# Kernel optimization log

Hardware: AMD Instinct MI355X
Metric: run time of the kernel (lower is better)

## Reference

```python
import jax, jax.numpy as jnp
import numpy as np

SIZES = [128, 64, 32, 16, 8]   # H=W per pyramid level
REFINE = 2                     # gather/refine level -> 32x32
C = 256
GROUPS = 32                    # dim_out // 8
EPS = 1e-5


def _maxpool(x, k):
    # exact adaptive_max_pool2d when input size is divisible by output size
    if k == 1:
        return x
    return jax.lax.reduce_window(x, -jnp.inf, jax.lax.max,
                                 (1, 1, k, k), (1, 1, k, k), 'VALID')


def _upsample(x, f):
    # nearest-neighbor interpolate with exact integer scale factor
    if f == 1:
        return x
    return jnp.repeat(jnp.repeat(x, f, axis=2), f, axis=3)


def _conv1x1(x, w, b):
    return jnp.einsum('nchw,oc->nohw', x, w) + b[None, :, None, None]


def _group_norm(x, gamma, beta):
    n, c, h, w = x.shape
    xg = x.reshape(n, GROUPS, c // GROUPS, h, w)
    mu = xg.mean(axis=(2, 3, 4), keepdims=True)
    var = xg.var(axis=(2, 3, 4), keepdims=True)
    xg = (xg - mu) * jax.lax.rsqrt(var + EPS)
    return xg.reshape(n, c, h, w) * gamma[None, :, None, None] + beta[None, :, None, None]


def _nonlocal(x, g_w, g_b, th_w, th_b, ph_w, ph_b, out_w, out_b, gn_g, gn_b):
    n, c, h, w = x.shape
    N = h * w
    g_x = _conv1x1(x, g_w, g_b).reshape(n, c, N)       # [n,c,N]
    th_x = _conv1x1(x, th_w, th_b).reshape(n, c, N)
    ph_x = _conv1x1(x, ph_w, ph_b).reshape(n, c, N)
    # pairwise = theta^T @ phi / N  (dot_product mode, no softmax)
    pw = jnp.einsum('nci,ncj->nij', th_x, ph_x) / N    # [n,N,N]
    y = jnp.einsum('nij,ncj->nci', pw, g_x)            # [n,c,N]
    y = y.reshape(n, c, h, w)
    out = _group_norm(_conv1x1(y, out_w, out_b), gn_g, gn_b)
    return x + out


def reference(f0, f1, f2, f3, f4,
              g_w, g_b, th_w, th_b, ph_w, ph_b,
              out_w, out_b, gn_g, gn_b):
    feats = [f0, f1, f2, f3, f4]
    gs = SIZES[REFINE]
    gathered = []
    for i, f in enumerate(feats):
        if i < REFINE:
            gathered.append(_maxpool(f, SIZES[i] // gs))
        else:
            gathered.append(_upsample(f, gs // SIZES[i]))
    bsf = sum(gathered) / len(gathered)
    bsf = _nonlocal(bsf, g_w, g_b, th_w, th_b, ph_w, ph_b, out_w, out_b, gn_g, gn_b)
    outs = []
    for i, f in enumerate(feats):
        if i < REFINE:
            res = _upsample(bsf, SIZES[i] // gs)
        else:
            res = _maxpool(bsf, gs // SIZES[i])
        outs.append(res + f)
    return tuple(outs)


def setup_inputs() -> dict:
    key = jax.random.key(0)
    ks = jax.random.split(key, 16)
    inp = {}
    for i, s in enumerate(SIZES):
        inp[f'f{i}'] = jax.random.normal(ks[i], (4, C, s, s), dtype=jnp.float32)
    std = 0.01
    inp['g_w'] = jax.random.normal(ks[5], (C, C), dtype=jnp.float32) * std
    inp['g_b'] = jnp.zeros((C,), jnp.float32)
    inp['th_w'] = jax.random.normal(ks[6], (C, C), dtype=jnp.float32) * std
    inp['th_b'] = jnp.zeros((C,), jnp.float32)
    inp['ph_w'] = jax.random.normal(ks[7], (C, C), dtype=jnp.float32) * std
    inp['ph_b'] = jnp.zeros((C,), jnp.float32)
    inp['out_w'] = jax.random.normal(ks[8], (C, C), dtype=jnp.float32) * std
    inp['out_b'] = jnp.zeros((C,), jnp.float32)
    inp['gn_g'] = jnp.ones((C,), jnp.float32)
    inp['gn_b'] = jnp.zeros((C,), jnp.float32)
    return inp
```

## Files before the change

### kernel.cpp

```cpp
#include <hip/hip_runtime.h>

typedef __bf16 bf16x8 __attribute__((ext_vector_type(8)));
typedef float f32x4 __attribute__((ext_vector_type(4)));

#define OFF_BSF   0x000000
#define OFF_BSFT  0x400000
#define OFF_BSFB  0x600000
#define OFF_YT    0x600000
#define OFF_Z     0x800000
#define OFF_SBH   0xC00000
#define OFF_SBL   0xC80000
#define OFF_T0    0xD00000
#define OFF_OWB   0xE00000
#define OFF_GWT   0xE20000
#define OFF_PHT   0xE40000
#define OFF_THT   0xE60000
#define OFF_UB    0xE80000
#define OFF_VB    0xEA0000
#define OFF_UT    0xEC0000
#define OFF_RPART 0xEE0000
#define OFF_R     0xEF0000
#define OFF_UV    0xEF1000
#define OFF_V2P   0xEF1400
#define OFF_W2P   0xEF2400
#define OFF_S2    0xEF3400
#define OFF_CVEC  0xEF4000
#define OFF_STATS 0xEF9000
#define OFF_W2SP  0xEFA000

__global__ __launch_bounds__(256) void prep_k(
    const float* __restrict__ f0, const float* __restrict__ f1,
    const float* __restrict__ f2, const float* __restrict__ f3,
    const float* __restrict__ f4,
    const float* __restrict__ g_w, const float* __restrict__ ph_w,
    const float* __restrict__ th_w, const float* __restrict__ ow_w,
    const float* __restrict__ g_b, const float* __restrict__ ph_b,
    const float* __restrict__ th_b,
    char* __restrict__ ws)
{
  const int blk = blockIdx.x, t = threadIdx.x;
  __shared__ __attribute__((aligned(16))) union {
    __bf16 Lt[16][66];
    __bf16 T[64][72];
    float vec2[544];
  } sm;

  if (blk < 48) {
    const int w = blk >> 4, tl = blk & 15;
    const float* src = (w == 0) ? g_w : (w == 1) ? ph_w : th_w;
    __bf16* dst = (__bf16*)(ws + ((w == 0) ? OFF_GWT : (w == 1) ? OFF_PHT : OFF_THT));
    const int ti = (tl >> 2) * 64, tj = (tl & 3) * 64;
#pragma unroll
    for (int i = 0; i < 4; ++i) {
      int idx = i * 256 + t;
      int r = idx >> 4, c4 = (idx & 15) << 2;
      float4 v = *(const float4*)&src[(size_t)(ti + r) * 256 + tj + c4];
      sm.T[c4 + 0][r] = (__bf16)v.x;
      sm.T[c4 + 1][r] = (__bf16)v.y;
      sm.T[c4 + 2][r] = (__bf16)v.z;
      sm.T[c4 + 3][r] = (__bf16)v.w;
    }
    __syncthreads();
#pragma unroll
    for (int i = 0; i < 2; ++i) {
      int idx = i * 256 + t;
      int aa = idx >> 3, cc = (idx & 7) << 3;
      bf16x8 o = *(const bf16x8*)&sm.T[aa][cc];
      *(bf16x8*)&dst[(size_t)(tj + aa) * 256 + ti + cc] = o;
    }
  } else if (blk < 52) {
    const int r0 = (blk - 48) * 64;
    __bf16* owB = (__bf16*)(ws + OFF_OWB);
#pragma unroll
    for (int i = 0; i < 8; ++i) {
      int lin = i * 2048 + t * 8;
      size_t gidx = (size_t)r0 * 256 + lin;
      float4 v0 = *(const float4*)&ow_w[gidx];
      float4 v1 = *(const float4*)&ow_w[gidx + 4];
      bf16x8 o;
      o[0] = (__bf16)v0.x; o[1] = (__bf16)v0.y; o[2] = (__bf16)v0.z; o[3] = (__bf16)v0.w;
      o[4] = (__bf16)v1.x; o[5] = (__bf16)v1.y; o[6] = (__bf16)v1.z; o[7] = (__bf16)v1.w;
      *(bf16x8*)&owB[gidx] = o;
    }
  } else if (blk < 68) {
    const int q = blk - 52;
    const int r0 = q * 16;
    float* uv = (float*)(ws + OFF_UV);
    sm.vec2[t] = g_b[t];
    __syncthreads();
    const int rl = t >> 4;
    const int ci = (t & 15) * 16;
    const float* p = ow_w + (size_t)(r0 + rl) * 256 + ci;
    float acc = 0.f;
#pragma unroll
    for (int u = 0; u < 4; ++u) {
      float4 v = *(const float4*)(p + u * 4);
      acc += v.x * sm.vec2[ci + u * 4]     + v.y * sm.vec2[ci + u * 4 + 1]
           + v.z * sm.vec2[ci + u * 4 + 2] + v.w * sm.vec2[ci + u * 4 + 3];
    }
    __syncthreads();
    sm.vec2[256 + rl * 17 + (t & 15)] = acc;
    __syncthreads();
    if (t < 16) {
      float s = 0.f;
#pragma unroll
      for (int i = 0; i < 16; ++i) s += sm.vec2[256 + t * 17 + i];
      uv[r0 + t] = s;
    }
  } else if (blk < 72) {
    const int q = blk - 68, c0 = q * 64;
    float* v2p = (float*)(ws + OFF_V2P);
    if (t < 64) sm.vec2[t] = th_b[c0 + t];
    __syncthreads();
    float acc = 0.f;
#pragma unroll 8
    for (int c = 0; c < 64; ++c)
      acc += ph_w[(size_t)(c0 + c) * 256 + t] * sm.vec2[c];
    v2p[q * 256 + t] = acc;
  } else if (blk < 76) {
    const int q = blk - 72, c0 = q * 64;
    float* w2p = (float*)(ws + OFF_W2P);
    if (t < 64) sm.vec2[t] = ph_b[c0 + t];
    __syncthreads();
    float acc = 0.f;
#pragma unroll 8
    for (int c = 0; c < 64; ++c)
      acc += th_w[(size_t)(c0 + c) * 256 + t] * sm.vec2[c];
    w2p[q * 256 + t] = acc;
  } else if (blk == 76) {
    float* s2 = (float*)(ws + OFF_S2);
    if (t < 64) {
      float pa = ph_b[t] * th_b[t] + ph_b[64 + t] * th_b[64 + t]
               + ph_b[128 + t] * th_b[128 + t] + ph_b[192 + t] * th_b[192 + t];
#pragma unroll
      for (int off = 32; off; off >>= 1) pa += __shfl_down(pa, off);
      if (t == 0) s2[0] = pa;
    }
    ((float*)(ws + OFF_STATS))[t] = 0.f;
  } else if (blk == 77) {
    float* cvec = (float*)(ws + OFF_CVEC);
#pragma unroll
    for (int i = 0; i < 4; ++i) cvec[i * 256 + t] = 0.f;
  } else {
    const int g = blk - 78;
    float*  bsf   = (float*)(ws + OFF_BSF);
    __bf16* bsfT  = (__bf16*)(ws + OFF_BSFT);
    __bf16* bsfB  = (__bf16*)(ws + OFF_BSFB);
    float*  rpart = (float*)(ws + OFF_RPART);
    const int sblk = g & 15, cgrp = (g >> 4) & 15, b = g >> 8;
    const int c0 = cgrp * 16, s0 = sblk * 64;
    const int spl = t & 63, sp = s0 + spl;
    const int y = sp >> 5, x = sp & 31;
#pragma unroll
    for (int i = 0; i < 4; ++i) {
      const int cl = (t >> 6) + i * 4;
      const int nc = b * 256 + c0 + cl;

      const float* p0 = f0 + (size_t)nc * 16384 + (y * 4) * 128 + x * 4;
      float4 r0 = *(const float4*)(p0);
      float4 r1 = *(const float4*)(p0 + 128);
      float4 r2 = *(const float4*)(p0 + 256);
      float4 r3 = *(const float4*)(p0 + 384);
      float a  = fmaxf(fmaxf(r0.x, r0.y), fmaxf(r0.z, r0.w));
      float bb = fmaxf(fmaxf(r1.x, r1.y), fmaxf(r1.z, r1.w));
      float c  = fmaxf(fmaxf(r2.x, r2.y), fmaxf(r2.z, r2.w));
      float d  = fmaxf(fmaxf(r3.x, r3.y), fmaxf(r3.z, r3.w));
      float m0v = fmaxf(fmaxf(a, bb), fmaxf(c, d));

      const float* p1 = f1 + (size_t)nc * 4096 + (y * 2) * 64 + x * 2;
      float2 s0v = *(const float2*)(p1);
      float2 s1v = *(const float2*)(p1 + 64);
      float m1v = fmaxf(fmaxf(s0v.x, s0v.y), fmaxf(s1v.x, s1v.y));

      float v2 = f2[(size_t)nc * 1024 + sp];
      float v3 = f3[(size_t)nc * 256 + (y >> 1) * 16 + (x >> 1)];
      float v4 = f4[(size_t)nc * 64  + (y >> 2) * 8  + (x >> 2)];
      float val = (m0v + m1v + v2 + v3 + v4) * 0.2f;
      bsf[(size_t)nc * 1024 + sp]  = val;
      bsfB[(size_t)nc * 1024 + sp] = (__bf16)val;
      sm.Lt[cl][spl] = (__bf16)val;
      float rs = val;
#pragma unroll
      for (int off = 32; off; off >>= 1) rs += __shfl_down(rs, off);
      if (spl == 0) rpart[sblk * 1024 + nc] = rs;
    }
    __syncthreads();
#pragma unroll
    for (int i = 0; i < 4; ++i) {
      int linear = t + i * 256;
      int spl2 = linear >> 4, cl2 = linear & 15;
      bsfT[((size_t)b * 1024 + s0 + spl2) * 256 + c0 + cl2] = sm.Lt[cl2][spl2];
    }
  }
}

__device__ __forceinline__ void gemm_acc(
    const __bf16* __restrict__ A, const __bf16* __restrict__ B,
    const int K, const int m0, const int n0,
    __bf16 (*Al)[64][72], __bf16 (*Bl)[64][72],
    f32x4 acc[2][2])
{
  const int t = threadIdx.x;
  const int lane = t & 63, wv = t >> 6;
  const int wm = (wv & 1) * 32, wn = (wv >> 1) * 32;
  const int fr = lane & 15, lk = (lane >> 4) * 8;
  const int sr = t >> 2, sk = (t & 3) * 16;

  const __bf16* Ar = A + (size_t)(m0 + sr) * K + sk;
  const __bf16* Br = B + (size_t)(n0 + sr) * K + sk;

  bf16x8 ra0 = *(const bf16x8*)(Ar);
  bf16x8 ra1 = *(const bf16x8*)(Ar + 8);
  bf16x8 rb0 = *(const bf16x8*)(Br);
  bf16x8 rb1 = *(const bf16x8*)(Br + 8);

  const int nIter = K >> 6;
  int p = 0;
  for (int it = 0; it < nIter; ++it) {
    *(bf16x8*)&Al[p][sr][sk]     = ra0;
    *(bf16x8*)&Al[p][sr][sk + 8] = ra1;
    *(bf16x8*)&Bl[p][sr][sk]     = rb0;
    *(bf16x8*)&Bl[p][sr][sk + 8] = rb1;
    __syncthreads();
    if (it + 1 < nIter) {
      const __bf16* An = Ar + (size_t)(it + 1) * 64;
      const __bf16* Bn = Br + (size_t)(it + 1) * 64;
      ra0 = *(const bf16x8*)(An);
      ra1 = *(const bf16x8*)(An + 8);
      rb0 = *(const bf16x8*)(Bn);
      rb1 = *(const bf16x8*)(Bn + 8);
    }
#pragma unroll
    for (int kk = 0; kk < 64; kk += 32) {
      bf16x8 a0 = *(const bf16x8*)&Al[p][wm + fr][kk + lk];
      bf16x8 a1 = *(const bf16x8*)&Al[p][wm + 16 + fr][kk + lk];
      bf16x8 b0 = *(const bf16x8*)&Bl[p][wn + fr][kk + lk];
      bf16x8 b1 = *(const bf16x8*)&Bl[p][wn + 16 + fr][kk + lk];
      acc[0][0] = __builtin_amdgcn_mfma_f32_16x16x32_bf16(a0, b0, acc[0][0], 0, 0, 0);
      acc[0][1] = __builtin_amdgcn_mfma_f32_16x16x32_bf16(a0, b1, acc[0][1], 0, 0, 0);
      acc[1][0] = __builtin_amdgcn_mfma_f32_16x16x32_bf16(a1, b0, acc[1][0], 0, 0, 0);
      acc[1][1] = __builtin_amdgcn_mfma_f32_16x16x32_bf16(a1, b1, acc[1][1], 0, 0, 0);
    }
    __syncthreads();
    p ^= 1;
  }
}

__device__ __forceinline__ void store_bf16(
    __bf16* dst, int ldst, const f32x4 acc[2][2],
    int m0, int n0, int wm, int wn, int rbase, int fr)
{
#pragma unroll
  for (int i = 0; i < 2; ++i)
#pragma unroll
    for (int r = 0; r < 4; ++r) {
      int m = m0 + wm + i * 16 + rbase + r;
#pragma unroll
      for (int j = 0; j < 2; ++j) {
        int n = n0 + wn + j * 16 + fr;
        dst[(size_t)m * ldst + n] = (__bf16)acc[i][j][r];
      }
    }
}

#define ZERO_ACC(acc) \
  _Pragma("unroll") for (int i_ = 0; i_ < 2; ++i_) \
  _Pragma("unroll") for (int j_ = 0; j_ < 2; ++j_) \
    acc[i_][j_] = (f32x4){0.f, 0.f, 0.f, 0.f};

__global__ __launch_bounds__(256) void p0_k(char* __restrict__ ws)
{
  const int blk = blockIdx.x, t = threadIdx.x;
  __shared__ __attribute__((aligned(16))) __bf16 Al[2][64][72];
  __shared__ __attribute__((aligned(16))) __bf16 Bl[2][64][72];
  float* shf = (float*)(&Al[0][0][0]);

  const int lane = t & 63, wv = t >> 6;
  const int wm = (wv & 1) * 32, wn = (wv >> 1) * 32;
  const int fr = lane & 15, rbase = (lane >> 4) * 4;
  (void)lane; (void)wv;

  const __bf16* bsfB = (const __bf16*)(ws + OFF_BSFB);

  if (blk < 64) {
    const int b = blk >> 4, tl = blk & 15;
    const int m0 = (tl >> 2) * 64, n0 = (tl & 3) * 64;
    f32x4 acc[2][2]; ZERO_ACC(acc);
    gemm_acc(bsfB + (size_t)b * 262144, bsfB + (size_t)b * 262144,
             1024, m0, n0, Al, Bl, acc);
    __bf16* oh = (__bf16*)(ws + OFF_SBH) + (size_t)b * 65536;
    __bf16* ol = (__bf16*)(ws + OFF_SBL) + (size_t)b * 65536;
#pragma unroll
    for (int i = 0; i < 2; ++i)
#pragma unroll
      for (int r = 0; r < 4; ++r) {
        int m = m0 + wm + i * 16 + rbase + r;
#pragma unroll
        for (int j = 0; j < 2; ++j) {
          int n = n0 + wn + j * 16 + fr;
          float v = acc[i][j][r];
          __bf16 h = (__bf16)v;
          oh[(size_t)m * 256 + n] = h;
          ol[(size_t)m * 256 + n] = (__bf16)(v - (float)h);
        }
      }
  } else if (blk < 80) {
    const int tl = blk - 64;
    const int m0 = (tl >> 2) * 64, n0 = (tl & 3) * 64;
    f32x4 acc[2][2]; ZERO_ACC(acc);
    gemm_acc((const __bf16*)(ws + OFF_OWB), (const __bf16*)(ws + OFF_GWT),
             256, m0, n0, Al, Bl, acc);
    __bf16* ub = (__bf16*)(ws + OFF_UB);
    __bf16* ut = (__bf16*)(ws + OFF_UT);
#pragma unroll
    for (int i = 0; i < 2; ++i)
#pragma unroll
      for (int r = 0; r < 4; ++r) {
        int m = m0 + wm + i * 16 + rbase + r;
#pragma unroll
        for (int j = 0; j < 2; ++j) {
          int n = n0 + wn + j * 16 + fr;
          __bf16 v = (__bf16)acc[i][j][r];
          ub[(size_t)m * 256 + n] = v;
          ut[(size_t)n * 256 + m] = v;
        }
      }
  } else if (blk < 96) {
    const int tl = blk - 80;
    const int m0 = (tl >> 2) * 64, n0 = (tl & 3) * 64;
    f32x4 acc[2][2]; ZERO_ACC(acc);
    gemm_acc((const __bf16*)(ws + OFF_PHT), (const __bf16*)(ws + OFF_THT),
             256, m0, n0, Al, Bl, acc);
    store_bf16((__bf16*)(ws + OFF_VB), 256, acc, m0, n0, wm, wn, rbase, fr);
  } else if (blk == 96) {
    const float* rpart = (const float*)(ws + OFF_RPART);
    float* Rr = (float*)(ws + OFF_R);
#pragma unroll
    for (int j2 = 0; j2 < 4; ++j2) {
      int idx = t + j2 * 256;
      float s = 0.f;
#pragma unroll
      for (int k = 0; k < 16; ++k) s += rpart[k * 1024 + idx];
      Rr[idx] = s;
    }
  } else {
    const int q = blk - 97;
    const int half = q >> 4, idx = q & 15;
    const int b = idx >> 2, seg = (idx & 3) * 256;
    const int ch0 = half * 128;
    const float* w2p = (const float*)(ws + OFF_W2P);
    const float* bsf = (const float*)(ws + OFF_BSF);
    float* w2sp = (float*)(ws + OFF_W2SP);
    if (t < 128) {
      int c = ch0 + t;
      shf[t] = w2p[c] + w2p[256 + c] + w2p[512 + c] + w2p[768 + c];
    }
    __syncthreads();
    float acc = 0.f;
#pragma unroll 8
    for (int c = 0; c < 128; ++c)
      acc += shf[c] * bsf[((size_t)(b * 256 + ch0 + c)) * 1024 + seg + t];
    w2sp[half * 4096 + b * 1024 + seg + t] = acc;
  }
}

__global__ __launch_bounds__(256) void p1_k(char* __restrict__ ws)
{
  const int blk = blockIdx.x, t = threadIdx.x;
  __shared__ __attribute__((aligned(16))) __bf16 Al[2][64][72];
  __shared__ __attribute__((aligned(16))) __bf16 Bl[2][64][72];
  float* shf = (float*)(&Al[0][0][0]);

  const int lane = t & 63, wv = t >> 6;
  const int wm = (wv & 1) * 32, wn = (wv >> 1) * 32;
  const int fr = lane & 15, rbase = (lane >> 4) * 4;
  (void)lane; (void)wv;

  const __bf16* UB = (const __bf16*)(ws + OFF_UB);
  const float* Rr  = (const float*)(ws + OFF_R);
  const float* uv  = (const float*)(ws + OFF_UV);

  if (blk < 64) {
    const int b = blk >> 4, tl = blk & 15;
    const int m0 = (tl >> 2) * 64, n0 = (tl & 3) * 64;
    f32x4 acc[2][2]; ZERO_ACC(acc);
    gemm_acc(UB, (const __bf16*)(ws + OFF_SBH) + (size_t)b * 65536,
             256, m0, n0, Al, Bl, acc);
    gemm_acc(UB, (const __bf16*)(ws + OFF_SBL) + (size_t)b * 65536,
             256, m0, n0, Al, Bl, acc);
    shf[t] = Rr[b * 256 + t];
    __syncthreads();
    __bf16* od = (__bf16*)(ws + OFF_T0) + (size_t)b * 65536;
#pragma unroll
    for (int i = 0; i < 2; ++i)
#pragma unroll
      for (int r = 0; r < 4; ++r) {
        int m = m0 + wm + i * 16 + rbase + r;
        float uvm = uv[m];
#pragma unroll
        for (int j = 0; j < 2; ++j) {
          int n = n0 + wn + j * 16 + fr;
          od[(size_t)m * 256 + n] = (__bf16)(acc[i][j][r] + uvm * shf[n]);
        }
      }
  } else if (blk < 320) {
    const int q = blk - 64;
    const int b = q >> 6, tl = q & 63;
    const int m0 = (tl >> 2) * 64, n0 = (tl & 3) * 64;
    f32x4 acc[2][2]; ZERO_ACC(acc);
    gemm_acc((const __bf16*)(ws + OFF_BSFT) + (size_t)b * 262144,
             (const __bf16*)(ws + OFF_VB), 256, m0, n0, Al, Bl, acc);
    const float* v2p = (const float*)(ws + OFF_V2P);
    shf[t] = v2p[t] + v2p[256 + t] + v2p[512 + t] + v2p[768 + t];
    __syncthreads();
    __bf16* od = (__bf16*)(ws + OFF_YT) + (size_t)b * 262144;
#pragma unroll
    for (int i = 0; i < 2; ++i)
#pragma unroll
      for (int r = 0; r < 4; ++r) {
        int m = m0 + wm + i * 16 + rbase + r;
#pragma unroll
        for (int j = 0; j < 2; ++j) {
          int n = n0 + wn + j * 16 + fr;
          od[(size_t)m * 256 + n] = (__bf16)(acc[i][j][r] + shf[n]);
        }
      }
  } else {
    const int q = blk - 320;
    const int b = q >> 2, cc = (q & 3) * 64;
    const __bf16* UT = (const __bf16*)(ws + OFF_UT);
    float* cvec = (float*)(ws + OFF_CVEC);
    if (t < 64) shf[t] = Rr[b * 256 + cc + t];
    __syncthreads();
    float acc = 0.f;
#pragma unroll 8
    for (int c = 0; c < 64; ++c)
      acc += (float)UT[(size_t)(cc + c) * 256 + t] * shf[c];
    atomicAdd(&cvec[b * 256 + t], acc);
  }
}

__global__ __launch_bounds__(256) void p2_k(char* __restrict__ ws,
                                            const float* __restrict__ ow_b)
{
  const int blk = blockIdx.x, t = threadIdx.x;
  __shared__ __attribute__((aligned(16))) __bf16 Al[2][64][72];
  __shared__ __attribute__((aligned(16))) __bf16 Bl[2][64][72];
  float* shf = (float*)(&Al[0][0][0]);

  const int lane = t & 63, wv = t >> 6;
  const int wm = (wv & 1) * 32, wn = (wv >> 1) * 32;
  const int fr = lane & 15, rbase = (lane >> 4) * 4;

  const int b = blk >> 6, t6 = blk & 63;
  const int mt = t6 >> 4, nt = t6 & 15;
  const int m0 = mt * 64, n0 = nt * 64;
  (void)nt;

  f32x4 acc[2][2]; ZERO_ACC(acc);
  gemm_acc((const __bf16*)(ws + OFF_T0) + (size_t)b * 65536,
           (const __bf16*)(ws + OFF_YT) + (size_t)b * 262144,
           256, m0, n0, Al, Bl, acc);

  const float* uv   = (const float*)(ws + OFF_UV);
  const float* cvec = (const float*)(ws + OFF_CVEC);
  const float* w2sp = (const float*)(ws + OFF_W2SP);
  const float s2v   = *(const float*)(ws + OFF_S2);
  float* SRAW = (float*)(ws + OFF_STATS);
  float* zb = (float*)(ws + OFF_Z) + (size_t)b * 262144;

  float gs[2] = {0.f, 0.f}, gq[2] = {0.f, 0.f};
  int gidx[2];
  const float s1024 = 1.f / 1024.f;
#pragma unroll
  for (int i = 0; i < 2; ++i) {
    gidx[i] = (wm + i * 16 + rbase) >> 3;
#pragma unroll
    for (int r = 0; r < 4; ++r) {
      int m = m0 + wm + i * 16 + rbase + r;
      float coefm = uv[m] + cvec[b * 256 + m] * s1024;
      float qm = s2v * coefm + ow_b[m];
#pragma unroll
      for (int j = 0; j < 2; ++j) {
        int n = n0 + wn + j * 16 + fr;
        float w2n = w2sp[b * 1024 + n] + w2sp[4096 + b * 1024 + n];
        float v = acc[i][j][r] * s1024 + coefm * w2n + qm;
        zb[(size_t)m * 1024 + n] = v;
        gs[i] += v;
        gq[i] += v * v;
      }
    }
  }
  __syncthreads();
  if (t < 16) shf[t] = 0.f;
  __syncthreads();
#pragma unroll
  for (int i = 0; i < 2; ++i) {
    atomicAdd(&shf[gidx[i] * 2], gs[i]);
    atomicAdd(&shf[gidx[i] * 2 + 1], gq[i]);
  }
  __syncthreads();
  if (t < 16) {
    int g = mt * 8 + (t >> 1);
    atomicAdd(&SRAW[(b * 32 + g) * 2 + (t & 1)], shf[t]);
  }
}

__device__ __forceinline__ float4 gmix(float4 bz, float4 zz, float a, float c)
{
  float4 r;
  r.x = bz.x + zz.x * a + c;
  r.y = bz.y + zz.y * a + c;
  r.z = bz.z + zz.z * a + c;
  r.w = bz.w + zz.w * a + c;
  return r;
}
__device__ __forceinline__ float max4(float4 v)
{ return fmaxf(fmaxf(v.x, v.y), fmaxf(v.z, v.w)); }

__device__ __forceinline__ void gn_coeff(const float2* __restrict__ ST,
                                         const float* __restrict__ gamma,
                                         const float* __restrict__ beta,
                                         int b, int ch, float& a, float& c0)
{
  float2 sq = ST[b * 32 + (ch >> 3)];
  float mean = sq.x * (1.0f / 8192.0f);
  float var  = sq.y * (1.0f / 8192.0f) - mean * mean;
  float inv  = rsqrtf(var + 1e-5f);
  a  = inv * gamma[ch];
  c0 = beta[ch] - mean * a;
}

__global__ __launch_bounds__(256) void scat_k(
    const char* __restrict__ ws,
    const float* __restrict__ f0, const float* __restrict__ f1,
    const float* __restrict__ f2, const float* __restrict__ f3,
    const float* __restrict__ f4,
    const float* __restrict__ gamma, const float* __restrict__ beta,
    float* __restrict__ out)
{
  const float* Z = (const float*)(ws + OFF_Z);
  const float* BSF = (const float*)(ws + OFF_BSF);
  const float2* ST = (const float2*)(ws + OFF_STATS);
  const int i4 = blockIdx.x * 256 + threadIdx.x;

  if (i4 < 4194304) {
    const int l = i4 << 2;
    const int x = l & 127, yy = (l >> 7) & 127, nc = l >> 14;
    const int ch = nc & 255, b = nc >> 8;
    float a, c0; gn_coeff(ST, gamma, beta, b, ch, a, c0);
    size_t base = (size_t)nc * 1024 + ((yy >> 2) << 5) + (x >> 2);
    float v = BSF[base] + Z[base] * a + c0;
    float4 f = ((const float4*)f0)[i4];
    float4 o; o.x = f.x + v; o.y = f.y + v; o.z = f.z + v; o.w = f.w + v;
    ((float4*)out)[i4] = o;
  } else if (i4 < 5242880) {
    const int l4 = i4 - 4194304;
    const int l = l4 << 2;
    const int x = l & 63, yy = (l >> 6) & 63, nc = l >> 12;
    const int ch = nc & 255, b = nc >> 8;
    float a, c0; gn_coeff(ST, gamma, beta, b, ch, a, c0);
    size_t base = (size_t)nc * 1024 + ((yy >> 1) << 5) + (x >> 1);
    float v0 = BSF[base] + Z[base] * a + c0;
    float v1 = BSF[base + 1] + Z[base + 1] * a + c0;
    float4 f = ((const float4*)f1)[l4];
    float4 o; o.x = f.x + v0; o.y = f.y + v0; o.z = f.z + v1; o.w = f.w + v1;
    ((float4*)out)[i4] = o;
  } else if (i4 < 5505024) {
    const int l4 = i4 - 5242880;
    const int l = l4 << 2;
    const int nc = l >> 10, e = l & 1023;
    const int ch = nc & 255, b = nc >> 8;
    float a, c0; gn_coeff(ST, gamma, beta, b, ch, a, c0);
    size_t base = (size_t)nc * 1024 + e;
    float4 z4 = *(const float4*)&Z[base];
    float4 b4 = *(const float4*)&BSF[base];
    float4 v = gmix(b4, z4, a, c0);
    float4 f = ((const float4*)f2)[l4];
    float4 o; o.x = f.x + v.x; o.y = f.y + v.y; o.z = f.z + v.z; o.w = f.w + v.w;
    ((float4*)out)[i4] = o;
  } else if (i4 < 5570560) {
    const int l4 = i4 - 5505024;
    const int l = l4 << 2;
    const int x = l & 15, yy = (l >> 4) & 15, nc = l >> 8;
    const int ch = nc & 255, b = nc >> 8;
    float a, c0; gn_coeff(ST, gamma, beta, b, ch, a, c0);
    size_t base = (size_t)nc * 1024;
    const int p0 = (yy * 2) * 32 + (x * 2);
    float4 r0a = gmix(*(const float4*)&BSF[base + p0],      *(const float4*)&Z[base + p0],      a, c0);
    float4 r0b = gmix(*(const float4*)&BSF[base + p0 + 4],  *(const float4*)&Z[base + p0 + 4],  a, c0);
    float4 r1a = gmix(*(const float4*)&BSF[base + p0 + 32], *(const float4*)&Z[base + p0 + 32], a, c0);
    float4 r1b = gmix(*(const float4*)&BSF[base + p0 + 36], *(const float4*)&Z[base + p0 + 36], a, c0);
    float4 f = ((const float4*)f3)[l4];
    float4 o;
    o.x = f.x + fmaxf(fmaxf(r0a.x, r0a.y), fmaxf(r1a.x, r1a.y));
    o.y = f.y + fmaxf(fmaxf(r0a.z, r0a.w), fmaxf(r1a.z, r1a.w));
    o.z = f.z + fmaxf(fmaxf(r0b.x, r0b.y), fmaxf(r1b.x, r1b.y));
    o.w = f.w + fmaxf(fmaxf(r0b.z, r0b.w), fmaxf(r1b.z, r1b.w));
    ((float4*)out)[i4] = o;
  } else {
    const int l4 = i4 - 5570560;
    const int l = l4 << 2;
    const int x = l & 7, yy = (l >> 3) & 7, nc = l >> 6;
    const int ch = nc & 255, b = nc >> 8;
    float a, c0; gn_coeff(ST, gamma, beta, b, ch, a, c0);
    size_t base = (size_t)nc * 1024;
    float4 mx = {-3.4e38f, -3.4e38f, -3.4e38f, -3.4e38f};
#pragma unroll
    for (int r = 0; r < 4; ++r) {
      const float* zp = &Z[base + (size_t)(yy * 4 + r) * 32 + x * 4];
      const float* bp = &BSF[base + (size_t)(yy * 4 + r) * 32 + x * 4];
      float4 q0 = gmix(*(const float4*)(bp),      *(const float4*)(zp),      a, c0);
      float4 q1 = gmix(*(const float4*)(bp + 4),  *(const float4*)(zp + 4),  a, c0);
      float4 q2 = gmix(*(const float4*)(bp + 8),  *(const float4*)(zp + 8),  a, c0);
      float4 q3 = gmix(*(const float4*)(bp + 12), *(const float4*)(zp + 12), a, c0);
      mx.x = fmaxf(mx.x, max4(q0));
      mx.y = fmaxf(mx.y, max4(q1));
      mx.z = fmaxf(mx.z, max4(q2));
      mx.w = fmaxf(mx.w, max4(q3));
    }
    float4 f = ((const float4*)f4)[l4];
    float4 o; o.x = f.x + mx.x; o.y = f.y + mx.y; o.z = f.z + mx.z; o.w = f.w + mx.w;
    ((float4*)out)[i4] = o;
  }
}

extern "C" void kernel_launch(void* const* d_in, const int* in_sizes, int n_in,
                              void* d_out, int out_size, void* d_ws, size_t ws_size,
                              hipStream_t stream)
{
  (void)in_sizes; (void)n_in; (void)out_size; (void)ws_size;
  const float* f0   = (const float*)d_in[0];
  const float* f1   = (const float*)d_in[1];
  const float* f2   = (const float*)d_in[2];
  const float* f3   = (const float*)d_in[3];
  const float* f4   = (const float*)d_in[4];
  const float* g_w  = (const float*)d_in[5];
  const float* g_b  = (const float*)d_in[6];
  const float* th_w = (const float*)d_in[7];
  const float* th_b = (const float*)d_in[8];
  const float* ph_w = (const float*)d_in[9];
  const float* ph_b = (const float*)d_in[10];
  const float* ow_w = (const float*)d_in[11];
  const float* ow_b = (const float*)d_in[12];
  const float* gn_g = (const float*)d_in[13];
  const float* gn_b = (const float*)d_in[14];
  char* ws = (char*)d_ws;

  prep_k<<<1102, 256, 0, stream>>>(f0, f1, f2, f3, f4,
                                   g_w, ph_w, th_w, ow_w,
                                   g_b, ph_b, th_b, ws);
  p0_k<<<129, 256, 0, stream>>>(ws);
  p1_k<<<336, 256, 0, stream>>>(ws);
  p2_k<<<256, 256, 0, stream>>>(ws, ow_b);
  scat_k<<<21824, 256, 0, stream>>>(ws, f0, f1, f2, f3, f4, gn_g, gn_b,
                                    (float*)d_out);
}
```

Baseline: 85.36 us.

## Store bsf and pre-norm output intermediates in bf16 instead of fp32

Drops the fp32 copy of the gathered feature map and reads the existing bf16 copy in the w2sp reduction and the final scatter kernel. The pre-GroupNorm output Z is also written and read as bf16, so intermediate traffic in the last kernels is roughly halved. YT is moved to a new offset to avoid overlapping the bf16 buffers. The cost is reduced precision in the residual path and the GN input, which may increase error against the fp32 reference.

```diff
diff --git a/kernel.cpp b/kernel.cpp
--- a/kernel.cpp
+++ b/kernel.cpp
@@ -1,13 +1,12 @@
 #include <hip/hip_runtime.h>
 
 typedef __bf16 bf16x8 __attribute__((ext_vector_type(8)));
+typedef __bf16 bf16x4v __attribute__((ext_vector_type(4)));
 typedef float f32x4 __attribute__((ext_vector_type(4)));
 
-#define OFF_BSF   0x000000
 #define OFF_BSFT  0x400000
 #define OFF_BSFB  0x600000
-#define OFF_YT    0x600000
-#define OFF_Z     0x800000
+#define OFF_ZB    0x800000
 #define OFF_SBH   0xC00000
 #define OFF_SBL   0xC80000
 #define OFF_T0    0xD00000
@@ -27,6 +26,7 @@
 #define OFF_CVEC  0xEF4000
 #define OFF_STATS 0xEF9000
 #define OFF_W2SP  0xEFA000
+#define OFF_YT    0xF10000
 
 __global__ __launch_bounds__(256) void prep_k(
     const float* __restrict__ f0, const float* __restrict__ f1,
@@ -143,7 +143,6 @@
     for (int i = 0; i < 4; ++i) cvec[i * 256 + t] = 0.f;
   } else {
     const int g = blk - 78;
-    float*  bsf   = (float*)(ws + OFF_BSF);
     __bf16* bsfT  = (__bf16*)(ws + OFF_BSFT);
     __bf16* bsfB  = (__bf16*)(ws + OFF_BSFB);
     float*  rpart = (float*)(ws + OFF_RPART);
@@ -176,7 +175,6 @@
       float v3 = f3[(size_t)nc * 256 + (y >> 1) * 16 + (x >> 1)];
       float v4 = f4[(size_t)nc * 64  + (y >> 2) * 8  + (x >> 2)];
       float val = (m0v + m1v + v2 + v3 + v4) * 0.2f;
-      bsf[(size_t)nc * 1024 + sp]  = val;
       bsfB[(size_t)nc * 1024 + sp] = (__bf16)val;
       sm.Lt[cl][spl] = (__bf16)val;
       float rs = val;
@@ -349,7 +347,6 @@
     const int b = idx >> 2, seg = (idx & 3) * 256;
     const int ch0 = half * 128;
     const float* w2p = (const float*)(ws + OFF_W2P);
-    const float* bsf = (const float*)(ws + OFF_BSF);
     float* w2sp = (float*)(ws + OFF_W2SP);
     if (t < 128) {
       int c = ch0 + t;
@@ -359,7 +356,7 @@
     float acc = 0.f;
 #pragma unroll 8
     for (int c = 0; c < 128; ++c)
-      acc += shf[c] * bsf[((size_t)(b * 256 + ch0 + c)) * 1024 + seg + t];
+      acc += shf[c] * (float)bsfB[((size_t)(b * 256 + ch0 + c)) * 1024 + seg + t];
     w2sp[half * 4096 + b * 1024 + seg + t] = acc;
   }
 }
@@ -467,7 +464,7 @@
   const float* w2sp = (const float*)(ws + OFF_W2SP);
   const float s2v   = *(const float*)(ws + OFF_S2);
   float* SRAW = (float*)(ws + OFF_STATS);
-  float* zb = (float*)(ws + OFF_Z) + (size_t)b * 262144;
+  __bf16* zb = (__bf16*)(ws + OFF_ZB) + (size_t)b * 262144;
 
   float gs[2] = {0.f, 0.f}, gq[2] = {0.f, 0.f};
   int gidx[2];
@@ -485,7 +482,7 @@
         int n = n0 + wn + j * 16 + fr;
         float w2n = w2sp[b * 1024 + n] + w2sp[4096 + b * 1024 + n];
         float v = acc[i][j][r] * s1024 + coefm * w2n + qm;
-        zb[(size_t)m * 1024 + n] = v;
+        zb[(size_t)m * 1024 + n] = (__bf16)v;
         gs[i] += v;
         gq[i] += v * v;
       }
@@ -506,6 +503,11 @@
   }
 }
 
+__device__ __forceinline__ float4 b2f4(const __bf16* p)
+{
+  bf16x4v v = *(const bf16x4v*)p;
+  return (float4){(float)v[0], (float)v[1], (float)v[2], (float)v[3]};
+}
 __device__ __forceinline__ float4 gmix(float4 bz, float4 zz, float a, float c)
 {
   float4 r;
@@ -539,8 +541,8 @@
     const float* __restrict__ gamma, const float* __restrict__ beta,
     float* __restrict__ out)
 {
-  const float* Z = (const float*)(ws + OFF_Z);
-  const float* BSF = (const float*)(ws + OFF_BSF);
+  const __bf16* ZB  = (const __bf16*)(ws + OFF_ZB);
+  const __bf16* BSF = (const __bf16*)(ws + OFF_BSFB);
   const float2* ST = (const float2*)(ws + OFF_STATS);
   const int i4 = blockIdx.x * 256 + threadIdx.x;
 
@@ -550,7 +552,7 @@
     const int ch = nc & 255, b = nc >> 8;
     float a, c0; gn_coeff(ST, gamma, beta, b, ch, a, c0);
     size_t base = (size_t)nc * 1024 + ((yy >> 2) << 5) + (x >> 2);
-    float v = BSF[base] + Z[base] * a + c0;
+    float v = (float)BSF[base] + (float)ZB[base] * a + c0;
     float4 f = ((const float4*)f0)[i4];
     float4 o; o.x = f.x + v; o.y = f.y + v; o.z = f.z + v; o.w = f.w + v;
     ((float4*)out)[i4] = o;
@@ -561,8 +563,8 @@
     const int ch = nc & 255, b = nc >> 8;
     float a, c0; gn_coeff(ST, gamma, beta, b, ch, a, c0);
     size_t base = (size_t)nc * 1024 + ((yy >> 1) << 5) + (x >> 1);
-    float v0 = BSF[base] + Z[base] * a + c0;
-    float v1 = BSF[base + 1] + Z[base + 1] * a + c0;
+    float v0 = (float)BSF[base] + (float)ZB[base] * a + c0;
+    float v1 = (float)BSF[base + 1] + (float)ZB[base + 1] * a + c0;
     float4 f = ((const float4*)f1)[l4];
     float4 o; o.x = f.x + v0; o.y = f.y + v0; o.z = f.z + v1; o.w = f.w + v1;
     ((float4*)out)[i4] = o;
@@ -573,8 +575,8 @@
     const int ch = nc & 255, b = nc >> 8;
     float a, c0; gn_coeff(ST, gamma, beta, b, ch, a, c0);
     size_t base = (size_t)nc * 1024 + e;
-    float4 z4 = *(const float4*)&Z[base];
-    float4 b4 = *(const float4*)&BSF[base];
+    float4 z4 = b2f4(&ZB[base]);
+    float4 b4 = b2f4(&BSF[base]);
     float4 v = gmix(b4, z4, a, c0);
     float4 f = ((const float4*)f2)[l4];
     float4 o; o.x = f.x + v.x; o.y = f.y + v.y; o.z = f.z + v.z; o.w = f.w + v.w;
@@ -587,10 +589,10 @@
     float a, c0; gn_coeff(ST, gamma, beta, b, ch, a, c0);
     size_t base = (size_t)nc * 1024;
     const int p0 = (yy * 2) * 32 + (x * 2);
-    float4 r0a = gmix(*(const float4*)&BSF[base + p0],      *(const float4*)&Z[base + p0],      a, c0);
-    float4 r0b = gmix(*(const float4*)&BSF[base + p0 + 4],  *(const float4*)&Z[base + p0 + 4],  a, c0);
-    float4 r1a = gmix(*(const float4*)&BSF[base + p0 + 32], *(const float4*)&Z[base + p0 + 32], a, c0);
-    float4 r1b = gmix(*(const float4*)&BSF[base + p0 + 36], *(const float4*)&Z[base + p0 + 36], a, c0);
+    float4 r0a = gmix(b2f4(&BSF[base + p0]),      b2f4(&ZB[base + p0]),      a, c0);
+    float4 r0b = gmix(b2f4(&BSF[base + p0 + 4]),  b2f4(&ZB[base + p0 + 4]),  a, c0);
+    float4 r1a = gmix(b2f4(&BSF[base + p0 + 32]), b2f4(&ZB[base + p0 + 32]), a, c0);
+    float4 r1b = gmix(b2f4(&BSF[base + p0 + 36]), b2f4(&ZB[base + p0 + 36]), a, c0);
     float4 f = ((const float4*)f3)[l4];
     float4 o;
     o.x = f.x + fmaxf(fmaxf(r0a.x, r0a.y), fmaxf(r1a.x, r1a.y));
@@ -608,12 +610,11 @@
     float4 mx = {-3.4e38f, -3.4e38f, -3.4e38f, -3.4e38f};
 #pragma unroll
     for (int r = 0; r < 4; ++r) {
-      const float* zp = &Z[base + (size_t)(yy * 4 + r) * 32 + x * 4];
-      const float* bp = &BSF[base + (size_t)(yy * 4 + r) * 32 + x * 4];
-      float4 q0 = gmix(*(const float4*)(bp),      *(const float4*)(zp),      a, c0);
-      float4 q1 = gmix(*(const float4*)(bp + 4),  *(const float4*)(zp + 4),  a, c0);
-      float4 q2 = gmix(*(const float4*)(bp + 8),  *(const float4*)(zp + 8),  a, c0);
-      float4 q3 = gmix(*(const float4*)(bp + 12), *(const float4*)(zp + 12), a, c0);
+      size_t rb = base + (size_t)(yy * 4 + r) * 32 + x * 4;
+      float4 q0 = gmix(b2f4(&BSF[rb]),      b2f4(&ZB[rb]),      a, c0);
+      float4 q1 = gmix(b2f4(&BSF[rb + 4]),  b2f4(&ZB[rb + 4]),  a, c0);
+      float4 q2 = gmix(b2f4(&BSF[rb + 8]),  b2f4(&ZB[rb + 8]),  a, c0);
+      float4 q3 = gmix(b2f4(&BSF[rb + 12]), b2f4(&ZB[rb + 12]), a, c0);
       mx.x = fmaxf(mx.x, max4(q0));
       mx.y = fmaxf(mx.y, max4(q1));
       mx.z = fmaxf(mx.z, max4(q2));
```

Result: faster. 76.25 us (-10.7%).
